# Performance work log

Measured on AMD Instinct MI355X. Metric: run time of the kernel, lower is better.

The kernel has to match this reference:

```python
import jax, jax.numpy as jnp
import numpy as np

B, C, T = 8, 512, 1024
H = 8
D = C // H          # head_dim = 64
K = 64              # max_rel_dist
REL = 2 * K + 1     # 129


def setup_inputs() -> dict:
    key = jax.random.key(0)
    ks = jax.random.split(key, 12)
    s = 0.02
    return {
        "x": jax.random.normal(ks[0], (B, C, T), jnp.float32),
        "x_mask": jnp.ones((B, 1, T), jnp.float32),
        "W_q": jax.random.normal(ks[1], (C, C), jnp.float32) * s,
        "b_q": jnp.zeros((C,), jnp.float32),
        "W_k": jax.random.normal(ks[2], (C, C), jnp.float32) * s,
        "b_k": jnp.zeros((C,), jnp.float32),
        "W_v": jax.random.normal(ks[3], (C, C), jnp.float32) * s,
        "b_v": jnp.zeros((C,), jnp.float32),
        "W_o": jax.random.normal(ks[4], (C, C), jnp.float32) * s,
        "b_o": jnp.zeros((C,), jnp.float32),
        "emb_rel_k": jax.random.normal(ks[5], (REL, D), jnp.float32) * 0.01,
        "emb_rel_v": jax.random.normal(ks[6], (REL, D), jnp.float32) * 0.01,
    }


def _conv1x1(x, W, b):
    # Conv1d with kernel_size=1: (B,C,T) x (Cout,Cin) -> (B,Cout,T)
    return jnp.einsum("oc,bct->bot", W, x) + b[None, :, None]


def _shape_heads(x):
    # (B,C,T) -> (B,H,T,D)
    b = x.shape[0]
    return x.reshape(b, H, D, T).transpose(0, 1, 3, 2)


def reference(x, x_mask, W_q, b_q, W_k, b_k, W_v, b_v, W_o, b_o, emb_rel_k, emb_rel_v):
    q = _shape_heads(_conv1x1(x, W_q, b_q))  # (B,H,T,D)
    k = _shape_heads(_conv1x1(x, W_k, b_k))
    v = _shape_heads(_conv1x1(x, W_v, b_v))

    # relative position indices: clamp(j - i, -K, K) + K  -> (T,T)
    pos = jnp.arange(T)
    rel_idx = jnp.clip(pos[None, :] - pos[:, None], -K, K) + K

    # scores: scaled QK^T plus unscaled relative-key term (faithful to source)
    attn = jnp.einsum("bhid,bhjd->bhij", q, k) / (D ** 0.5)
    rel_k_tt = emb_rel_k[rel_idx]            # (T,T,D)
    attn = attn + jnp.einsum("bhid,ijd->bhij", q, rel_k_tt)

    # key mask: positions with x_mask <= 0 get -1e9
    key_mask = (x_mask <= 0).reshape(x.shape[0], 1, 1, T)
    attn = jnp.where(key_mask, -1e9, attn)
    attn = jax.nn.softmax(attn, axis=-1)     # dropout p=0.0 -> identity

    y = jnp.einsum("bhij,bhjd->bhid", attn, v)
    rel_v_tt = emb_rel_v[rel_idx]            # (T,T,D)
    y = y + jnp.einsum("bhij,ijd->bhid", attn, rel_v_tt)

    # (B,H,T,D) -> (B,H,D,T) -> (B,C,T)
    y = y.transpose(0, 1, 3, 2).reshape(x.shape[0], C, T)
    y = _conv1x1(y, W_o, b_o)
    return y * x_mask
```

## Files before the change

### kernel.cpp

```cpp
#include <hip/hip_runtime.h>

#define B_   8
#define C_   512
#define T_   1024
#define H_   8
#define D_   64
#define K_   64
#define REL_ 129

typedef unsigned short u16;
typedef __attribute__((ext_vector_type(8))) short short8;
typedef __attribute__((ext_vector_type(4))) float f32x4;

__device__ __forceinline__ float b2f(u16 u) {
    return __uint_as_float(((unsigned)u) << 16);
}
__device__ __forceinline__ u16 f2b(float f) {
    unsigned x = __float_as_uint(f);
    x += 0x7fffu + ((x >> 16) & 1u);
    return (u16)(x >> 16);
}

__global__ __launch_bounds__(256) void cast_x_kernel(
    const float* __restrict__ x, u16* __restrict__ xt)
{
    __shared__ u16 tile[64][72];
    const int t0 = blockIdx.x * 64, c0 = blockIdx.y * 64, b = blockIdx.z;
    const int tid = threadIdx.x;
    const int f = tid & 15, r0 = tid >> 4;
#pragma unroll
    for (int p = 0; p < 4; ++p) {
        const int c = r0 + p * 16;
        const float4 v = *(const float4*)(x + ((size_t)b * C_ + c0 + c) * T_ + t0 + f * 4);
        tile[c][f * 4 + 0] = f2b(v.x);
        tile[c][f * 4 + 1] = f2b(v.y);
        tile[c][f * 4 + 2] = f2b(v.z);
        tile[c][f * 4 + 3] = f2b(v.w);
    }
    __syncthreads();
#pragma unroll
    for (int p = 0; p < 4; ++p) {
        const int t = r0 + p * 16;
        ushort4 u;
        u.x = tile[f * 4 + 0][t];
        u.y = tile[f * 4 + 1][t];
        u.z = tile[f * 4 + 2][t];
        u.w = tile[f * 4 + 3][t];
        *(ushort4*)(xt + ((size_t)b * T_ + t0 + t) * C_ + c0 + f * 4) = u;
    }
}

__global__ __launch_bounds__(256) void cast_w_kernel(
    const float* __restrict__ Wq, const float* __restrict__ Wk,
    const float* __restrict__ Wv, const float* __restrict__ Wo,
    u16* __restrict__ Wh)
{
    const int gid = blockIdx.x * 256 + threadIdx.x;
    const int s = gid >> 16;
    const int off = (gid & 65535) * 4;
    const float* W = (s == 0) ? Wq : (s == 1) ? Wk : (s == 2) ? Wv : Wo;
    const float4 v = *(const float4*)(W + off);
    ushort4 u;
    u.x = f2b(v.x); u.y = f2b(v.y); u.z = f2b(v.z); u.w = f2b(v.w);
    *(ushort4*)(Wh + ((size_t)s << 18) + off) = u;
}

__global__ __launch_bounds__(256) void cast_rel_kernel(
    const float* __restrict__ erk, const float* __restrict__ erv,
    u16* __restrict__ ervt, u16* __restrict__ erkb)
{
    const int idx = blockIdx.x * 256 + threadIdx.x;
    if (idx < 64 * 160) {
        const int d = idx / 160, rel = idx % 160;
        ervt[idx] = (rel < REL_) ? f2b(erv[rel * D_ + d]) : (u16)0;
    } else {
        const int j = idx - 64 * 160;
        if (j < REL_ * D_) erkb[j] = f2b(erk[j]);
    }
}

__global__ __launch_bounds__(256) void proj_mfma(
    const u16* __restrict__ xt, const u16* __restrict__ Wh,
    const float* __restrict__ bq, const float* __restrict__ bk, const float* __restrict__ bv,
    u16* __restrict__ qh, u16* __restrict__ kh, u16* __restrict__ vt)
{
    __shared__ u16 Wt[64][72];

    const int t0 = blockIdx.x * 64;
    const int h  = blockIdx.y;
    const int sel = blockIdx.z >> 3;
    const int b   = blockIdx.z & 7;
    const int tid = threadIdx.x, wave = tid >> 6, lane = tid & 63;
    const int quad = lane >> 4, l16 = lane & 15;

    const u16* Wbase = Wh + ((size_t)sel << 18) + ((size_t)(h * 64) << 9);
    const u16* A = xt + (((size_t)b * T_ + t0 + wave * 16 + l16) << 9);

    const int so = tid >> 2;
    const int sc = (tid & 3) * 16;
    const u16* wsrc = Wbase + ((size_t)so << 9) + sc;

    f32x4 acc[4] = {{0.f,0.f,0.f,0.f},{0.f,0.f,0.f,0.f},{0.f,0.f,0.f,0.f},{0.f,0.f,0.f,0.f}};

    uint4 wv0 = *(const uint4*)(wsrc);
    uint4 wv1 = *(const uint4*)(wsrc + 8);
#pragma unroll 1
    for (int i = 0; i < 8; ++i) {
        const int c0 = i * 64;
        __syncthreads();
        *(uint4*)&Wt[so][sc] = wv0;
        *(uint4*)&Wt[so][sc + 8] = wv1;
        __syncthreads();
        if (i < 7) {
            wv0 = *(const uint4*)(wsrc + c0 + 64);
            wv1 = *(const uint4*)(wsrc + c0 + 72);
        }
#pragma unroll
        for (int kk = 0; kk < 64; kk += 32) {
            const short8 af = *(const short8*)(A + c0 + kk + quad * 8);
#pragma unroll
            for (int nt = 0; nt < 4; ++nt) {
                const short8 bf = *(const short8*)(&Wt[nt * 16 + l16][kk + quad * 8]);
                acc[nt] = __builtin_amdgcn_mfma_f32_16x16x32_bf16(af, bf, acc[nt], 0, 0, 0);
            }
        }
    }

    const float* bias = (sel == 0) ? bq : (sel == 1) ? bk : bv;
    const int bh = b * 8 + h;
#pragma unroll
    for (int nt = 0; nt < 4; ++nt) {
        const int d = nt * 16 + l16;
        const float bo = bias[h * 64 + d];
#pragma unroll
        for (int rix = 0; rix < 4; ++rix) {
            const int t = t0 + wave * 16 + quad * 4 + rix;
            const u16 val = f2b(acc[nt][rix] + bo);
            if (sel == 2) {
                vt[(((size_t)bh * 64 + d) << 10) + t] = val;
            } else {
                u16* dst = sel ? kh : qh;
                dst[(((size_t)bh * T_ + t) << 6) + d] = val;
            }
        }
    }
}

__global__ __launch_bounds__(256, 2) void attn_kernel(
    const u16* __restrict__ qh, const u16* __restrict__ kh, const u16* __restrict__ vt,
    const u16* __restrict__ erkb, const u16* __restrict__ ervt,
    const float* __restrict__ xmask, u16* __restrict__ yf)
{
    __shared__ u16   Sb[32][1032];
    __shared__ u16   sw[32][168];
    __shared__ float red[4][32][2];
    __shared__ float invrow[32];

    const int gid = blockIdx.x;
    const int x8 = gid & 7, r5 = gid >> 3;
    const int bh = x8 + 8 * (r5 >> 5);
    const int i0 = (r5 & 31) * 32;
    const int b = bh >> 3, h = bh & 7;
    const int tid = threadIdx.x, wave = tid >> 6, lane = tid & 63;
    const int quad = lane >> 4, l16 = lane & 15;

    short8 qa[2][2];
#pragma unroll
    for (int g = 0; g < 2; ++g) {
        const u16* qrow = qh + (((size_t)bh * T_ + i0 + g * 16 + l16) << 6);
        qa[g][0] = *(const short8*)(qrow + quad * 8);
        qa[g][1] = *(const short8*)(qrow + 32 + quad * 8);
    }

    for (int tile = wave; tile < 9; tile += 4) {
        const int rel = tile * 16 + l16;
        const int rl = rel > 128 ? 128 : rel;
        const u16* ep = erkb + rl * 64 + quad * 8;
        const short8 b0 = *(const short8*)(ep);
        const short8 b1 = *(const short8*)(ep + 32);
#pragma unroll
        for (int g = 0; g < 2; ++g) {
            f32x4 m = {0.f, 0.f, 0.f, 0.f};
            m = __builtin_amdgcn_mfma_f32_16x16x32_bf16(qa[g][0], b0, m, 0, 0, 0);
            m = __builtin_amdgcn_mfma_f32_16x16x32_bf16(qa[g][1], b1, m, 0, 0, 0);
            if (rel < 129) {
#pragma unroll
                for (int rix = 0; rix < 4; ++rix)
                    sw[g * 16 + quad * 4 + rix][rel] = f2b(m[rix]);
            }
        }
    }
    __syncthreads();

    float psum[2][4] = {{0.f,0.f,0.f,0.f},{0.f,0.f,0.f,0.f}};
    float phi [2][4] = {{0.f,0.f,0.f,0.f},{0.f,0.f,0.f,0.f}};
    float slo_c[2][4], shi_c[2][4];
#pragma unroll
    for (int g = 0; g < 2; ++g)
#pragma unroll
        for (int rix = 0; rix < 4; ++rix) {
            const int row = g * 16 + quad * 4 + rix;
            slo_c[g][rix] = b2f(sw[row][0]);
            shi_c[g][rix] = b2f(sw[row][2 * K_]);
        }
    {
        const u16* kb = kh + ((size_t)bh << 16);
#pragma unroll
        for (int ct = 0; ct < 16; ++ct) {
            const int j0 = wave * 256 + ct * 16;
            const u16* krow = kb + ((size_t)(j0 + l16) << 6);
            const short8 kb0 = *(const short8*)(krow + quad * 8);
            const short8 kb1 = *(const short8*)(krow + 32 + quad * 8);
            const int j = j0 + l16;
            const float xmv = xmask[b * T_ + j];
#pragma unroll
            for (int g = 0; g < 2; ++g) {
                f32x4 acc = {0.f, 0.f, 0.f, 0.f};
                acc = __builtin_amdgcn_mfma_f32_16x16x32_bf16(qa[g][0], kb0, acc, 0, 0, 0);
                acc = __builtin_amdgcn_mfma_f32_16x16x32_bf16(qa[g][1], kb1, acc, 0, 0, 0);
                const int dd = j0 - (i0 + g * 16);
                if (dd <= -79) {
#pragma unroll
                    for (int rix = 0; rix < 4; ++rix) {
                        const int row = g * 16 + quad * 4 + rix;
                        float val = acc[rix] * 0.125f + slo_c[g][rix];
                        val = (xmv > 0.f) ? val : -1e9f;
                        const u16 pb = f2b(__expf(fminf(val, 30.f)));
                        const float er = b2f(pb);
                        Sb[row][j] = pb;
                        psum[g][rix] += er;
                    }
                } else if (dd >= 79) {
#pragma unroll
                    for (int rix = 0; rix < 4; ++rix) {
                        const int row = g * 16 + quad * 4 + rix;
                        float val = acc[rix] * 0.125f + shi_c[g][rix];
                        val = (xmv > 0.f) ? val : -1e9f;
                        const u16 pb = f2b(__expf(fminf(val, 30.f)));
                        const float er = b2f(pb);
                        Sb[row][j] = pb;
                        psum[g][rix] += er;
                        phi[g][rix]  += er;
                    }
                } else {
#pragma unroll
                    for (int rix = 0; rix < 4; ++rix) {
                        const int row = g * 16 + quad * 4 + rix;
                        const int i = i0 + row;
                        int rel = j - i;
                        rel = (rel < -K_) ? -K_ : (rel > K_) ? K_ : rel;
                        float val = acc[rix] * 0.125f + b2f(sw[row][rel + K_]);
                        val = (xmv > 0.f) ? val : -1e9f;
                        const u16 pb = f2b(__expf(fminf(val, 30.f)));
                        const float er = b2f(pb);
                        Sb[row][j] = pb;
                        psum[g][rix] += er;
                        phi[g][rix]  += (j >= i + K_) ? er : 0.f;
                    }
                }
            }
        }
#pragma unroll
        for (int m = 1; m < 16; m <<= 1)
#pragma unroll
            for (int g = 0; g < 2; ++g)
#pragma unroll
                for (int rix = 0; rix < 4; ++rix) {
                    psum[g][rix] += __shfl_xor(psum[g][rix], m);
                    phi[g][rix]  += __shfl_xor(phi[g][rix], m);
                }
        if (l16 == 0)
#pragma unroll
            for (int g = 0; g < 2; ++g)
#pragma unroll
                for (int rix = 0; rix < 4; ++rix) {
                    const int row = g * 16 + quad * 4 + rix;
                    red[wave][row][0] = psum[g][rix];
                    red[wave][row][1] = phi[g][rix];
                }
    }
    __syncthreads();

    {
        const int rr = tid >> 3;
        const int c0 = tid & 7;
        const float sumrow = red[0][rr][0] + red[1][rr][0] + red[2][rr][0] + red[3][rr][0];
        const float phirow = red[0][rr][1] + red[1][rr][1] + red[2][rr][1] + red[3][rr][1];
        float intsum = 0.f;
        for (int rel = c0; rel < 168; rel += 8) {
            if (rel == 0 || rel == 2 * K_) continue;
            u16 v = 0;
            if (rel < 2 * K_) {
                const int j = i0 + rr + rel - K_;
                if (j >= 0 && j < T_) v = Sb[rr][j];
                intsum += b2f(v);
            }
            sw[rr][rel] = v;
        }
        intsum += __shfl_xor(intsum, 1);
        intsum += __shfl_xor(intsum, 2);
        intsum += __shfl_xor(intsum, 4);
        if (c0 == 0) {
            sw[rr][2 * K_] = f2b(phirow);
            sw[rr][0]      = f2b(sumrow - intsum - phirow);
            invrow[rr]     = 1.0f / sumrow;
        }
    }
    __syncthreads();

    {
        const int dh = wave * 16 + l16;
        const u16* vb = vt + ((size_t)bh << 16) + ((size_t)dh << 10);
        f32x4 og0 = {0.f, 0.f, 0.f, 0.f}, og1 = {0.f, 0.f, 0.f, 0.f};
#pragma unroll 4
        for (int ks = 0; ks < 32; ++ks) {
            const short8 af = *(const short8*)(vb + (ks << 5) + quad * 8);
            const short8 p0 = *(const short8*)(&Sb[l16][ks * 32 + quad * 8]);
            const short8 p1 = *(const short8*)(&Sb[16 + l16][ks * 32 + quad * 8]);
            og0 = __builtin_amdgcn_mfma_f32_16x16x32_bf16(af, p0, og0, 0, 0, 0);
            og1 = __builtin_amdgcn_mfma_f32_16x16x32_bf16(af, p1, og1, 0, 0, 0);
        }
        const u16* ep = ervt + dh * 160;
#pragma unroll
        for (int kt = 0; kt < 5; ++kt) {
            const short8 af = *(const short8*)(ep + kt * 32 + quad * 8);
            const short8 p0 = *(const short8*)(&sw[l16][kt * 32 + quad * 8]);
            const short8 p1 = *(const short8*)(&sw[16 + l16][kt * 32 + quad * 8]);
            og0 = __builtin_amdgcn_mfma_f32_16x16x32_bf16(af, p0, og0, 0, 0, 0);
            og1 = __builtin_amdgcn_mfma_f32_16x16x32_bf16(af, p1, og1, 0, 0, 0);
        }
        const float iv0 = invrow[l16];
        const float iv1 = invrow[16 + l16];
        const int dbase = (h << 6) + wave * 16 + quad * 4;
        ushort4 u0, u1;
        u0.x = f2b(og0[0] * iv0); u0.y = f2b(og0[1] * iv0);
        u0.z = f2b(og0[2] * iv0); u0.w = f2b(og0[3] * iv0);
        u1.x = f2b(og1[0] * iv1); u1.y = f2b(og1[1] * iv1);
        u1.z = f2b(og1[2] * iv1); u1.w = f2b(og1[3] * iv1);
        *(ushort4*)(yf + (((size_t)b * T_ + i0 + l16) << 9) + dbase) = u0;
        *(ushort4*)(yf + (((size_t)b * T_ + i0 + 16 + l16) << 9) + dbase) = u1;
    }
}

__global__ __launch_bounds__(256) void outproj_mfma(
    const u16* __restrict__ yf, const u16* __restrict__ Woh, const float* __restrict__ bo,
    const float* __restrict__ xmask, float* __restrict__ out)
{
    __shared__ u16 Yt[64][72];

    const int o0 = blockIdx.x * 64;
    const int b  = blockIdx.y >> 4;
    const int t0 = (blockIdx.y & 15) * 64;
    const int tid = threadIdx.x, wave = tid >> 6, lane = tid & 63;
    const int quad = lane >> 4, l16 = lane & 15;

    const u16* A = Woh + ((size_t)(o0 + wave * 16 + l16) << 9);

    const int so = tid >> 2;
    const int sc = (tid & 3) * 16;
    const u16* ysrc = yf + (((size_t)b * T_ + t0 + so) << 9) + sc;

    f32x4 acc[4] = {{0.f,0.f,0.f,0.f},{0.f,0.f,0.f,0.f},{0.f,0.f,0.f,0.f},{0.f,0.f,0.f,0.f}};

    uint4 wv0 = *(const uint4*)(ysrc);
    uint4 wv1 = *(const uint4*)(ysrc + 8);
#pragma unroll 1
    for (int i = 0; i < 8; ++i) {
        const int c0 = i * 64;
        __syncthreads();
        *(uint4*)&Yt[so][sc] = wv0;
        *(uint4*)&Yt[so][sc + 8] = wv1;
        __syncthreads();
        if (i < 7) {
            wv0 = *(const uint4*)(ysrc + c0 + 64);
            wv1 = *(const uint4*)(ysrc + c0 + 72);
        }
#pragma unroll
        for (int kk = 0; kk < 64; kk += 32) {
            const short8 af = *(const short8*)(A + c0 + kk + quad * 8);
#pragma unroll
            for (int nt = 0; nt < 4; ++nt) {
                const short8 bf = *(const short8*)(&Yt[nt * 16 + l16][kk + quad * 8]);
                acc[nt] = __builtin_amdgcn_mfma_f32_16x16x32_bf16(af, bf, acc[nt], 0, 0, 0);
            }
        }
    }

#pragma unroll
    for (int nt = 0; nt < 4; ++nt) {
        const int t = t0 + nt * 16 + l16;
        const float xmv = xmask[b * T_ + t];
#pragma unroll
        for (int rix = 0; rix < 4; ++rix) {
            const int o = o0 + wave * 16 + quad * 4 + rix;
            out[((size_t)b * C_ + o) * T_ + t] = (acc[nt][rix] + bo[o]) * xmv;
        }
    }
}

extern "C" void kernel_launch(void* const* d_in, const int* in_sizes, int n_in,
                              void* d_out, int out_size, void* d_ws, size_t ws_size,
                              hipStream_t stream) {
    const float* x     = (const float*)d_in[0];
    const float* xmask = (const float*)d_in[1];
    const float* Wq    = (const float*)d_in[2];
    const float* bq    = (const float*)d_in[3];
    const float* Wk    = (const float*)d_in[4];
    const float* bk    = (const float*)d_in[5];
    const float* Wv    = (const float*)d_in[6];
    const float* bv    = (const float*)d_in[7];
    const float* Wo    = (const float*)d_in[8];
    const float* bo    = (const float*)d_in[9];
    const float* erk   = (const float*)d_in[10];
    const float* erv   = (const float*)d_in[11];

    const size_t need = 44077184;
    if (ws_size < need) return;
    u16* xt   = (u16*)d_ws;
    u16* Wh   = (u16*)((char*)d_ws + 8388608);
    u16* qh   = (u16*)((char*)d_ws + 10485760);
    u16* kh   = (u16*)((char*)d_ws + 18874368);
    u16* vt   = (u16*)((char*)d_ws + 27262976);
    u16* yf   = (u16*)((char*)d_ws + 35651584);
    u16* ervt = (u16*)((char*)d_ws + 44040192);
    u16* erkb = (u16*)((char*)d_ws + 44060672);
    float* out = (float*)d_out;

    cast_x_kernel<<<dim3(T_ / 64, C_ / 64, B_), 256, 0, stream>>>(x, xt);
    cast_w_kernel<<<dim3(1024), 256, 0, stream>>>(Wq, Wk, Wv, Wo, Wh);
    cast_rel_kernel<<<dim3(73), 256, 0, stream>>>(erk, erv, ervt, erkb);
    proj_mfma<<<dim3(T_ / 64, H_, 3 * B_), 256, 0, stream>>>(
        xt, Wh, bq, bk, bv, qh, kh, vt);
    attn_kernel<<<dim3(2048), 256, 0, stream>>>(
        qh, kh, vt, erkb, ervt, xmask, yf);
    outproj_mfma<<<dim3(C_ / 64, B_ * (T_ / 64)), 256, 0, stream>>>(
        yf, Wh + ((size_t)3 << 18), bo, xmask, out);
}
```

Measured before the change: 249.5 us.

## Retile projection GEMMs to 128x128 and shrink attention row tile to 16

The QKV and output projection kernels move from 64x64 tiles with A read straight from global memory to 128x128 tiles, staging both operands in shared memory, with each wave computing a 4x4 grid of MFMA tiles. This raises operand reuse and cuts global traffic per FLOP, at the cost of more registers and fewer blocks. The attention kernel now handles 16 query rows per block instead of 32, which halves shared memory and allows 4 blocks per CU for better occupancy. In exchange, K/V and relative-embedding loads are reused across fewer rows, so more of that traffic is redundant.

```diff
diff --git a/kernel.cpp b/kernel.cpp
--- a/kernel.cpp
+++ b/kernel.cpp
@@ -84,93 +84,119 @@
     const float* __restrict__ bq, const float* __restrict__ bk, const float* __restrict__ bv,
     u16* __restrict__ qh, u16* __restrict__ kh, u16* __restrict__ vt)
 {
-    __shared__ u16 Wt[64][72];
-
-    const int t0 = blockIdx.x * 64;
-    const int h  = blockIdx.y;
+    __shared__ u16 As[128][72];
+    __shared__ u16 Bs[128][72];
+
+    const int t0 = blockIdx.x * 128;
+    const int oy = blockIdx.y;
     const int sel = blockIdx.z >> 3;
     const int b   = blockIdx.z & 7;
     const int tid = threadIdx.x, wave = tid >> 6, lane = tid & 63;
     const int quad = lane >> 4, l16 = lane & 15;
-
-    const u16* Wbase = Wh + ((size_t)sel << 18) + ((size_t)(h * 64) << 9);
-    const u16* A = xt + (((size_t)b * T_ + t0 + wave * 16 + l16) << 9);
-
-    const int so = tid >> 2;
-    const int sc = (tid & 3) * 16;
-    const u16* wsrc = Wbase + ((size_t)so << 9) + sc;
-
-    f32x4 acc[4] = {{0.f,0.f,0.f,0.f},{0.f,0.f,0.f,0.f},{0.f,0.f,0.f,0.f},{0.f,0.f,0.f,0.f}};
-
-    uint4 wv0 = *(const uint4*)(wsrc);
-    uint4 wv1 = *(const uint4*)(wsrc + 8);
+    const int wr = wave >> 1, wc = wave & 1;
+
+    const u16* Abase = xt + (((size_t)b * T_ + t0) << 9);
+    const u16* Bbase = Wh + ((size_t)sel << 18) + (((size_t)oy * 128) << 9);
+
+    int srow[4], scol[4];
+#pragma unroll
+    for (int p = 0; p < 4; ++p) {
+        const int idx = p * 256 + tid;
+        srow[p] = idx >> 3;
+        scol[p] = (idx & 7) * 8;
+    }
+
+    f32x4 acc[4][4];
+#pragma unroll
+    for (int mi = 0; mi < 4; ++mi)
+#pragma unroll
+        for (int ni = 0; ni < 4; ++ni) acc[mi][ni] = (f32x4){0.f, 0.f, 0.f, 0.f};
+
+    uint4 ra[4], rb[4];
+#pragma unroll
+    for (int p = 0; p < 4; ++p) {
+        ra[p] = *(const uint4*)(Abase + ((size_t)srow[p] << 9) + scol[p]);
+        rb[p] = *(const uint4*)(Bbase + ((size_t)srow[p] << 9) + scol[p]);
+    }
 #pragma unroll 1
-    for (int i = 0; i < 8; ++i) {
-        const int c0 = i * 64;
+    for (int kt = 0; kt < 8; ++kt) {
         __syncthreads();
-        *(uint4*)&Wt[so][sc] = wv0;
-        *(uint4*)&Wt[so][sc + 8] = wv1;
+#pragma unroll
+        for (int p = 0; p < 4; ++p) {
+            *(uint4*)&As[srow[p]][scol[p]] = ra[p];
+            *(uint4*)&Bs[srow[p]][scol[p]] = rb[p];
+        }
         __syncthreads();
-        if (i < 7) {
-            wv0 = *(const uint4*)(wsrc + c0 + 64);
-            wv1 = *(const uint4*)(wsrc + c0 + 72);
+        if (kt < 7) {
+            const int cn = (kt + 1) * 64;
+#pragma unroll
+            for (int p = 0; p < 4; ++p) {
+                ra[p] = *(const uint4*)(Abase + ((size_t)srow[p] << 9) + cn + scol[p]);
+                rb[p] = *(const uint4*)(Bbase + ((size_t)srow[p] << 9) + cn + scol[p]);
+            }
         }
 #pragma unroll
         for (int kk = 0; kk < 64; kk += 32) {
-            const short8 af = *(const short8*)(A + c0 + kk + quad * 8);
-#pragma unroll
-            for (int nt = 0; nt < 4; ++nt) {
-                const short8 bf = *(const short8*)(&Wt[nt * 16 + l16][kk + quad * 8]);
-                acc[nt] = __builtin_amdgcn_mfma_f32_16x16x32_bf16(af, bf, acc[nt], 0, 0, 0);
-            }
+            short8 af[4], bf[4];
+#pragma unroll
+            for (int mi = 0; mi < 4; ++mi)
+                af[mi] = *(const short8*)(&As[wr * 64 + mi * 16 + l16][kk + quad * 8]);
+#pragma unroll
+            for (int ni = 0; ni < 4; ++ni)
+                bf[ni] = *(const short8*)(&Bs[wc * 64 + ni * 16 + l16][kk + quad * 8]);
+#pragma unroll
+            for (int mi = 0; mi < 4; ++mi)
+#pragma unroll
+                for (int ni = 0; ni < 4; ++ni)
+                    acc[mi][ni] = __builtin_amdgcn_mfma_f32_16x16x32_bf16(af[mi], bf[ni], acc[mi][ni], 0, 0, 0);
         }
     }
 
     const float* bias = (sel == 0) ? bq : (sel == 1) ? bk : bv;
+    const int h = oy * 2 + wc;
     const int bh = b * 8 + h;
 #pragma unroll
-    for (int nt = 0; nt < 4; ++nt) {
-        const int d = nt * 16 + l16;
+    for (int ni = 0; ni < 4; ++ni) {
+        const int d = ni * 16 + l16;
         const float bo = bias[h * 64 + d];
 #pragma unroll
-        for (int rix = 0; rix < 4; ++rix) {
-            const int t = t0 + wave * 16 + quad * 4 + rix;
-            const u16 val = f2b(acc[nt][rix] + bo);
-            if (sel == 2) {
-                vt[(((size_t)bh * 64 + d) << 10) + t] = val;
-            } else {
-                u16* dst = sel ? kh : qh;
-                dst[(((size_t)bh * T_ + t) << 6) + d] = val;
-            }
-        }
-    }
-}
-
-__global__ __launch_bounds__(256, 2) void attn_kernel(
+        for (int mi = 0; mi < 4; ++mi) {
+#pragma unroll
+            for (int rix = 0; rix < 4; ++rix) {
+                const int t = t0 + wr * 64 + mi * 16 + quad * 4 + rix;
+                const u16 val = f2b(acc[mi][ni][rix] + bo);
+                if (sel == 2) {
+                    vt[(((size_t)bh * 64 + d) << 10) + t] = val;
+                } else {
+                    u16* dst = sel ? kh : qh;
+                    dst[(((size_t)bh * T_ + t) << 6) + d] = val;
+                }
+            }
+        }
+    }
+}
+
+__global__ __launch_bounds__(256, 4) void attn_kernel(
     const u16* __restrict__ qh, const u16* __restrict__ kh, const u16* __restrict__ vt,
     const u16* __restrict__ erkb, const u16* __restrict__ ervt,
     const float* __restrict__ xmask, u16* __restrict__ yf)
 {
-    __shared__ u16   Sb[32][1032];
-    __shared__ u16   sw[32][168];
-    __shared__ float red[4][32][2];
-    __shared__ float invrow[32];
+    __shared__ u16   Sb[16][1032];
+    __shared__ u16   sw[16][168];
+    __shared__ float red[4][16][2];
+    __shared__ float invrow[16];
 
     const int gid = blockIdx.x;
-    const int x8 = gid & 7, r5 = gid >> 3;
-    const int bh = x8 + 8 * (r5 >> 5);
-    const int i0 = (r5 & 31) * 32;
+    const int x8 = gid & 7, idx = gid >> 3;
+    const int bh = x8 + 8 * (idx >> 6);
+    const int i0 = (idx & 63) * 16;
     const int b = bh >> 3, h = bh & 7;
     const int tid = threadIdx.x, wave = tid >> 6, lane = tid & 63;
     const int quad = lane >> 4, l16 = lane & 15;
 
-    short8 qa[2][2];
-#pragma unroll
-    for (int g = 0; g < 2; ++g) {
-        const u16* qrow = qh + (((size_t)bh * T_ + i0 + g * 16 + l16) << 6);
-        qa[g][0] = *(const short8*)(qrow + quad * 8);
-        qa[g][1] = *(const short8*)(qrow + 32 + quad * 8);
-    }
+    const u16* qrow = qh + (((size_t)bh * T_ + i0 + l16) << 6);
+    const short8 qa0 = *(const short8*)(qrow + quad * 8);
+    const short8 qa1 = *(const short8*)(qrow + 32 + quad * 8);
 
     for (int tile = wave; tile < 9; tile += 4) {
         const int rel = tile * 16 + l16;
@@ -178,31 +204,25 @@
         const u16* ep = erkb + rl * 64 + quad * 8;
         const short8 b0 = *(const short8*)(ep);
         const short8 b1 = *(const short8*)(ep + 32);
-#pragma unroll
-        for (int g = 0; g < 2; ++g) {
-            f32x4 m = {0.f, 0.f, 0.f, 0.f};
-            m = __builtin_amdgcn_mfma_f32_16x16x32_bf16(qa[g][0], b0, m, 0, 0, 0);
-            m = __builtin_amdgcn_mfma_f32_16x16x32_bf16(qa[g][1], b1, m, 0, 0, 0);
-            if (rel < 129) {
-#pragma unroll
-                for (int rix = 0; rix < 4; ++rix)
-                    sw[g * 16 + quad * 4 + rix][rel] = f2b(m[rix]);
-            }
+        f32x4 m = {0.f, 0.f, 0.f, 0.f};
+        m = __builtin_amdgcn_mfma_f32_16x16x32_bf16(qa0, b0, m, 0, 0, 0);
+        m = __builtin_amdgcn_mfma_f32_16x16x32_bf16(qa1, b1, m, 0, 0, 0);
+        if (rel < 129) {
+#pragma unroll
+            for (int rix = 0; rix < 4; ++rix) sw[quad * 4 + rix][rel] = f2b(m[rix]);
         }
     }
     __syncthreads();
 
-    float psum[2][4] = {{0.f,0.f,0.f,0.f},{0.f,0.f,0.f,0.f}};
-    float phi [2][4] = {{0.f,0.f,0.f,0.f},{0.f,0.f,0.f,0.f}};
-    float slo_c[2][4], shi_c[2][4];
-#pragma unroll
-    for (int g = 0; g < 2; ++g)
-#pragma unroll
-        for (int rix = 0; rix < 4; ++rix) {
-            const int row = g * 16 + quad * 4 + rix;
-            slo_c[g][rix] = b2f(sw[row][0]);
-            shi_c[g][rix] = b2f(sw[row][2 * K_]);
-        }
+    float psum[4] = {0.f, 0.f, 0.f, 0.f};
+    float phi [4] = {0.f, 0.f, 0.f, 0.f};
+    float slo_c[4], shi_c[4];
+#pragma unroll
+    for (int rix = 0; rix < 4; ++rix) {
+        const int row = quad * 4 + rix;
+        slo_c[rix] = b2f(sw[row][0]);
+        shi_c[rix] = b2f(sw[row][2 * K_]);
+    }
     {
         const u16* kb = kh + ((size_t)bh << 16);
 #pragma unroll
@@ -213,81 +233,74 @@
             const short8 kb1 = *(const short8*)(krow + 32 + quad * 8);
             const int j = j0 + l16;
             const float xmv = xmask[b * T_ + j];
-#pragma unroll
-            for (int g = 0; g < 2; ++g) {
-                f32x4 acc = {0.f, 0.f, 0.f, 0.f};
-                acc = __builtin_amdgcn_mfma_f32_16x16x32_bf16(qa[g][0], kb0, acc, 0, 0, 0);
-                acc = __builtin_amdgcn_mfma_f32_16x16x32_bf16(qa[g][1], kb1, acc, 0, 0, 0);
-                const int dd = j0 - (i0 + g * 16);
-                if (dd <= -79) {
-#pragma unroll
-                    for (int rix = 0; rix < 4; ++rix) {
-                        const int row = g * 16 + quad * 4 + rix;
-                        float val = acc[rix] * 0.125f + slo_c[g][rix];
-                        val = (xmv > 0.f) ? val : -1e9f;
-                        const u16 pb = f2b(__expf(fminf(val, 30.f)));
-                        const float er = b2f(pb);
-                        Sb[row][j] = pb;
-                        psum[g][rix] += er;
-                    }
-                } else if (dd >= 79) {
-#pragma unroll
-                    for (int rix = 0; rix < 4; ++rix) {
-                        const int row = g * 16 + quad * 4 + rix;
-                        float val = acc[rix] * 0.125f + shi_c[g][rix];
-                        val = (xmv > 0.f) ? val : -1e9f;
-                        const u16 pb = f2b(__expf(fminf(val, 30.f)));
-                        const float er = b2f(pb);
-                        Sb[row][j] = pb;
-                        psum[g][rix] += er;
-                        phi[g][rix]  += er;
-                    }
-                } else {
-#pragma unroll
-                    for (int rix = 0; rix < 4; ++rix) {
-                        const int row = g * 16 + quad * 4 + rix;
-                        const int i = i0 + row;
-                        int rel = j - i;
-                        rel = (rel < -K_) ? -K_ : (rel > K_) ? K_ : rel;
-                        float val = acc[rix] * 0.125f + b2f(sw[row][rel + K_]);
-                        val = (xmv > 0.f) ? val : -1e9f;
-                        const u16 pb = f2b(__expf(fminf(val, 30.f)));
-                        const float er = b2f(pb);
-                        Sb[row][j] = pb;
-                        psum[g][rix] += er;
-                        phi[g][rix]  += (j >= i + K_) ? er : 0.f;
-                    }
+            f32x4 acc = {0.f, 0.f, 0.f, 0.f};
+            acc = __builtin_amdgcn_mfma_f32_16x16x32_bf16(qa0, kb0, acc, 0, 0, 0);
+            acc = __builtin_amdgcn_mfma_f32_16x16x32_bf16(qa1, kb1, acc, 0, 0, 0);
+            const int dd = j0 - i0;
+            if (dd <= -79) {
+#pragma unroll
+                for (int rix = 0; rix < 4; ++rix) {
+                    const int row = quad * 4 + rix;
+                    float val = acc[rix] * 0.125f + slo_c[rix];
+                    val = (xmv > 0.f) ? val : -1e9f;
+                    const u16 pb = f2b(__expf(fminf(val, 30.f)));
+                    const float er = b2f(pb);
+                    Sb[row][j] = pb;
+                    psum[rix] += er;
                 }
+            } else if (dd >= 79) {
+#pragma unroll
+                for (int rix = 0; rix < 4; ++rix) {
+                    const int row = quad * 4 + rix;
+                    float val = acc[rix] * 0.125f + shi_c[rix];
+                    val = (xmv > 0.f) ? val : -1e9f;
+                    const u16 pb = f2b(__expf(fminf(val, 30.f)));
+                    const float er = b2f(pb);
+                    Sb[row][j] = pb;
+                    psum[rix] += er;
+                    phi[rix]  += er;
+                }
+            } else {
+#pragma unroll
+                for (int rix = 0; rix < 4; ++rix) {
+                    const int row = quad * 4 + rix;
+                    const int i = i0 + row;
+                    int rel = j - i;
+                    rel = (rel < -K_) ? -K_ : (rel > K_) ? K_ : rel;
+                    float val = acc[rix] * 0.125f + b2f(sw[row][rel + K_]);
+                    val = (xmv > 0.f) ? val : -1e9f;
+                    const u16 pb = f2b(__expf(fminf(val, 30.f)));
+                    const float er = b2f(pb);
+                    Sb[row][j] = pb;
+                    psum[rix] += er;
+                    phi[rix]  += (j >= i + K_) ? er : 0.f;
+                }
             }
         }
 #pragma unroll
         for (int m = 1; m < 16; m <<= 1)
 #pragma unroll
-            for (int g = 0; g < 2; ++g)
-#pragma unroll
-                for (int rix = 0; rix < 4; ++rix) {
-                    psum[g][rix] += __shfl_xor(psum[g][rix], m);
-                    phi[g][rix]  += __shfl_xor(phi[g][rix], m);
-                }
+            for (int rix = 0; rix < 4; ++rix) {
+                psum[rix] += __shfl_xor(psum[rix], m);
+                phi[rix]  += __shfl_xor(phi[rix], m);
+            }
         if (l16 == 0)
 #pragma unroll
-            for (int g = 0; g < 2; ++g)
-#pragma unroll
-                for (int rix = 0; rix < 4; ++rix) {
-                    const int row = g * 16 + quad * 4 + rix;
-                    red[wave][row][0] = psum[g][rix];
-                    red[wave][row][1] = phi[g][rix];
-                }
+            for (int rix = 0; rix < 4; ++rix) {
+                const int row = quad * 4 + rix;
+                red[wave][row][0] = psum[rix];
+                red[wave][row][1] = phi[rix];
+            }
     }
     __syncthreads();
 
     {
-        const int rr = tid >> 3;
-        const int c0 = tid & 7;
+        const int rr = tid >> 4;
+        const int c0 = tid & 15;
         const float sumrow = red[0][rr][0] + red[1][rr][0] + red[2][rr][0] + red[3][rr][0];
         const float phirow = red[0][rr][1] + red[1][rr][1] + red[2][rr][1] + red[3][rr][1];
         float intsum = 0.f;
-        for (int rel = c0; rel < 168; rel += 8) {
+        for (int rel = c0; rel < 168; rel += 16) {
             if (rel == 0 || rel == 2 * K_) continue;
             u16 v = 0;
             if (rel < 2 * K_) {
@@ -300,6 +313,7 @@
         intsum += __shfl_xor(intsum, 1);
         intsum += __shfl_xor(intsum, 2);
         intsum += __shfl_xor(intsum, 4);
+        intsum += __shfl_xor(intsum, 8);
         if (c0 == 0) {
             sw[rr][2 * K_] = f2b(phirow);
             sw[rr][0]      = f2b(sumrow - intsum - phirow);
@@ -311,34 +325,25 @@
     {
         const int dh = wave * 16 + l16;
         const u16* vb = vt + ((size_t)bh << 16) + ((size_t)dh << 10);
-        f32x4 og0 = {0.f, 0.f, 0.f, 0.f}, og1 = {0.f, 0.f, 0.f, 0.f};
+        f32x4 og = {0.f, 0.f, 0.f, 0.f};
 #pragma unroll 4
         for (int ks = 0; ks < 32; ++ks) {
             const short8 af = *(const short8*)(vb + (ks << 5) + quad * 8);
             const short8 p0 = *(const short8*)(&Sb[l16][ks * 32 + quad * 8]);
-            const short8 p1 = *(const short8*)(&Sb[16 + l16][ks * 32 + quad * 8]);
-            og0 = __builtin_amdgcn_mfma_f32_16x16x32_bf16(af, p0, og0, 0, 0, 0);
-            og1 = __builtin_amdgcn_mfma_f32_16x16x32_bf16(af, p1, og1, 0, 0, 0);
+            og = __builtin_amdgcn_mfma_f32_16x16x32_bf16(af, p0, og, 0, 0, 0);
         }
         const u16* ep = ervt + dh * 160;
 #pragma unroll
         for (int kt = 0; kt < 5; ++kt) {
             const short8 af = *(const short8*)(ep + kt * 32 + quad * 8);
             const short8 p0 = *(const short8*)(&sw[l16][kt * 32 + quad * 8]);
-            const short8 p1 = *(const short8*)(&sw[16 + l16][kt * 32 + quad * 8]);
-            og0 = __builtin_amdgcn_mfma_f32_16x16x32_bf16(af, p0, og0, 0, 0, 0);
-            og1 = __builtin_amdgcn_mfma_f32_16x16x32_bf16(af, p1, og1, 0, 0, 0);
-        }
-        const float iv0 = invrow[l16];
-        const float iv1 = invrow[16 + l16];
-        const int dbase = (h << 6) + wave * 16 + quad * 4;
-        ushort4 u0, u1;
-        u0.x = f2b(og0[0] * iv0); u0.y = f2b(og0[1] * iv0);
-        u0.z = f2b(og0[2] * iv0); u0.w = f2b(og0[3] * iv0);
-        u1.x = f2b(og1[0] * iv1); u1.y = f2b(og1[1] * iv1);
-        u1.z = f2b(og1[2] * iv1); u1.w = f2b(og1[3] * iv1);
-        *(ushort4*)(yf + (((size_t)b * T_ + i0 + l16) << 9) + dbase) = u0;
-        *(ushort4*)(yf + (((size_t)b * T_ + i0 + 16 + l16) << 9) + dbase) = u1;
+            og = __builtin_amdgcn_mfma_f32_16x16x32_bf16(af, p0, og, 0, 0, 0);
+        }
+        const float iv = invrow[l16];
+        ushort4 u0;
+        u0.x = f2b(og[0] * iv); u0.y = f2b(og[1] * iv);
+        u0.z = f2b(og[2] * iv); u0.w = f2b(og[3] * iv);
+        *(ushort4*)(yf + (((size_t)b * T_ + i0 + l16) << 9) + (h << 6) + wave * 16 + quad * 4) = u0;
     }
 }
 
@@ -346,54 +351,84 @@
     const u16* __restrict__ yf, const u16* __restrict__ Woh, const float* __restrict__ bo,
     const float* __restrict__ xmask, float* __restrict__ out)
 {
-    __shared__ u16 Yt[64][72];
-
-    const int o0 = blockIdx.x * 64;
-    const int b  = blockIdx.y >> 4;
-    const int t0 = (blockIdx.y & 15) * 64;
+    __shared__ u16 As[128][72];
+    __shared__ u16 Bs[128][72];
+
+    const int o0 = blockIdx.x * 128;
+    const int t0 = blockIdx.y * 128;
+    const int b  = blockIdx.z;
     const int tid = threadIdx.x, wave = tid >> 6, lane = tid & 63;
     const int quad = lane >> 4, l16 = lane & 15;
-
-    const u16* A = Woh + ((size_t)(o0 + wave * 16 + l16) << 9);
-
-    const int so = tid >> 2;
-    const int sc = (tid & 3) * 16;
-    const u16* ysrc = yf + (((size_t)b * T_ + t0 + so) << 9) + sc;
-
-    f32x4 acc[4] = {{0.f,0.f,0.f,0.f},{0.f,0.f,0.f,0.f},{0.f,0.f,0.f,0.f},{0.f,0.f,0.f,0.f}};
-
-    uint4 wv0 = *(const uint4*)(ysrc);
-    uint4 wv1 = *(const uint4*)(ysrc + 8);
+    const int wr = wave >> 1, wc = wave & 1;
+
+    const u16* Abase = Woh + ((size_t)o0 << 9);
+    const u16* Bbase = yf + (((size_t)b * T_ + t0) << 9);
+
+    int srow[4], scol[4];
+#pragma unroll
+    for (int p = 0; p < 4; ++p) {
+        const int idx = p * 256 + tid;
+        srow[p] = idx >> 3;
+        scol[p] = (idx & 7) * 8;
+    }
+
+    f32x4 acc[4][4];
+#pragma unroll
+    for (int mi = 0; mi < 4; ++mi)
+#pragma unroll
+        for (int ni = 0; ni < 4; ++ni) acc[mi][ni] = (f32x4){0.f, 0.f, 0.f, 0.f};
+
+    uint4 ra[4], rb[4];
+#pragma unroll
+    for (int p = 0; p < 4; ++p) {
+        ra[p] = *(const uint4*)(Abase + ((size_t)srow[p] << 9) + scol[p]);
+        rb[p] = *(const uint4*)(Bbase + ((size_t)srow[p] << 9) + scol[p]);
+    }
 #pragma unroll 1
-    for (int i = 0; i < 8; ++i) {
-        const int c0 = i * 64;
+    for (int kt = 0; kt < 8; ++kt) {
         __syncthreads();
-        *(uint4*)&Yt[so][sc] = wv0;
-        *(uint4*)&Yt[so][sc + 8] = wv1;
+#pragma unroll
+        for (int p = 0; p < 4; ++p) {
+            *(uint4*)&As[srow[p]][scol[p]] = ra[p];
+            *(uint4*)&Bs[srow[p]][scol[p]] = rb[p];
+        }
         __syncthreads();
-        if (i < 7) {
-            wv0 = *(const uint4*)(ysrc + c0 + 64);
-            wv1 = *(const uint4*)(ysrc + c0 + 72);
+        if (kt < 7) {
+            const int cn = (kt + 1) * 64;
+#pragma unroll
+            for (int p = 0; p < 4; ++p) {
+                ra[p] = *(const uint4*)(Abase + ((size_t)srow[p] << 9) + cn + scol[p]);
+                rb[p] = *(const uint4*)(Bbase + ((size_t)srow[p] << 9) + cn + scol[p]);
+            }
         }
 #pragma unroll
         for (int kk = 0; kk < 64; kk += 32) {
-            const short8 af = *(const short8*)(A + c0 + kk + quad * 8);
-#pragma unroll
-            for (int nt = 0; nt < 4; ++nt) {
-                const short8 bf = *(const short8*)(&Yt[nt * 16 + l16][kk + quad * 8]);
-                acc[nt] = __builtin_amdgcn_mfma_f32_16x16x32_bf16(af, bf, acc[nt], 0, 0, 0);
-            }
-        }
-    }
-
-#pragma unroll
-    for (int nt = 0; nt < 4; ++nt) {
-        const int t = t0 + nt * 16 + l16;
+            short8 af[4], bf[4];
+#pragma unroll
+            for (int mi = 0; mi < 4; ++mi)
+                af[mi] = *(const short8*)(&As[wr * 64 + mi * 16 + l16][kk + quad * 8]);
+#pragma unroll
+            for (int ni = 0; ni < 4; ++ni)
+                bf[ni] = *(const short8*)(&Bs[wc * 64 + ni * 16 + l16][kk + quad * 8]);
+#pragma unroll
+            for (int mi = 0; mi < 4; ++mi)
+#pragma unroll
+                for (int ni = 0; ni < 4; ++ni)
+                    acc[mi][ni] = __builtin_amdgcn_mfma_f32_16x16x32_bf16(af[mi], bf[ni], acc[mi][ni], 0, 0, 0);
+        }
+    }
+
+#pragma unroll
+    for (int ni = 0; ni < 4; ++ni) {
+        const int t = t0 + wc * 64 + ni * 16 + l16;
         const float xmv = xmask[b * T_ + t];
 #pragma unroll
-        for (int rix = 0; rix < 4; ++rix) {
-            const int o = o0 + wave * 16 + quad * 4 + rix;
-            out[((size_t)b * C_ + o) * T_ + t] = (acc[nt][rix] + bo[o]) * xmv;
+        for (int mi = 0; mi < 4; ++mi) {
+#pragma unroll
+            for (int rix = 0; rix < 4; ++rix) {
+                const int o = o0 + wr * 64 + mi * 16 + quad * 4 + rix;
+                out[(((size_t)(b * C_ + o)) << 10) + t] = (acc[mi][ni][rix] + bo[o]) * xmv;
+            }
         }
     }
 }
@@ -429,10 +464,10 @@
     cast_x_kernel<<<dim3(T_ / 64, C_ / 64, B_), 256, 0, stream>>>(x, xt);
     cast_w_kernel<<<dim3(1024), 256, 0, stream>>>(Wq, Wk, Wv, Wo, Wh);
     cast_rel_kernel<<<dim3(73), 256, 0, stream>>>(erk, erv, ervt, erkb);
-    proj_mfma<<<dim3(T_ / 64, H_, 3 * B_), 256, 0, stream>>>(
+    proj_mfma<<<dim3(T_ / 128, 4, 3 * B_), 256, 0, stream>>>(
         xt, Wh, bq, bk, bv, qh, kh, vt);
-    attn_kernel<<<dim3(2048), 256, 0, stream>>>(
+    attn_kernel<<<dim3(4096), 256, 0, stream>>>(
         qh, kh, vt, erkb, ervt, xmask, yf);
-    outproj_mfma<<<dim3(C_ / 64, B_ * (T_ / 64)), 256, 0, stream>>>(
+    outproj_mfma<<<dim3(4, 8, B_), 256, 0, stream>>>(
         yf, Wh + ((size_t)3 << 18), bo, xmask, out);
 }
```

Result: slower. 348.7 us (+39.8%).
